# Performance work log

Measured on AMD Instinct MI355X. Metric: run time of the kernel, lower is better.

The kernel has to match this reference:

```python
import jax, jax.numpy as jnp
import numpy as np

INPUT_SIZE = 1024
HIDDEN_SIZE = 1024
SEQ_LEN = 512
BATCH = 64


def setup_inputs() -> dict:
    key = jax.random.key(0)
    ks = jax.random.split(key, 9)
    I, H = INPUT_SIZE, HIDDEN_SIZE
    s3 = 1.0 / np.sqrt(I + 2 * H)  # torch nn.Linear default init scale
    s2 = 1.0 / np.sqrt(I + H)
    return {
        "x": jax.random.normal(ks[0], (SEQ_LEN, BATCH, I), dtype=jnp.float32),
        "hidden": jnp.zeros((BATCH, H), dtype=jnp.float32),
        "cell": jnp.zeros((BATCH, H), dtype=jnp.float32),
        "W_write": jax.random.uniform(ks[1], (H, I + 2 * H), minval=-s3, maxval=s3),
        "b_write": jax.random.uniform(ks[2], (H,), minval=-s3, maxval=s3),
        "W_forget": jax.random.uniform(ks[3], (H, I + 2 * H), minval=-s3, maxval=s3),
        "b_forget": jax.random.uniform(ks[4], (H,), minval=-s3, maxval=s3),
        "W_cell": jax.random.uniform(ks[5], (H, I + H), minval=-s2, maxval=s2),
        "b_cell": jax.random.uniform(ks[6], (H,), minval=-s2, maxval=s2),
        "W_output": jax.random.uniform(ks[7], (H, I + 2 * H), minval=-s3, maxval=s3),
        "b_output": jax.random.uniform(ks[8], (H,), minval=-s3, maxval=s3),
    }


def reference(x, hidden, cell, W_write, b_write, W_forget, b_forget,
              W_cell, b_cell, W_output, b_output):
    # Peephole-style LSTM: write/forget gates see (x, h, c); candidate sees
    # (x, h); output gate sees (x, h, c_new). Sequential over time via scan.
    def step(carry, x_t):
        h, c = carry
        comb_xhc = jnp.concatenate([x_t, h, c], axis=-1)          # [B, I+2H]
        w = jax.nn.sigmoid(comb_xhc @ W_write.T + b_write)        # write gate
        f = jax.nn.sigmoid(comb_xhc @ W_forget.T + b_forget)      # forget gate
        comb_xh = jnp.concatenate([x_t, h], axis=-1)              # [B, I+H]
        c_new = f * c + w * jnp.tanh(comb_xh @ W_cell.T + b_cell)
        comb_new = jnp.concatenate([x_t, h, c_new], axis=-1)
        o = jax.nn.sigmoid(comb_new @ W_output.T + b_output)      # output gate
        h_new = o * jnp.tanh(c_new)
        return (h_new, c_new), h_new

    (h_f, c_f), outputs = jax.lax.scan(step, (hidden, cell), x)
    return outputs, (h_f, c_f)
```

## Files before the change

### kernel.cpp

```cpp
#include <hip/hip_runtime.h>
#include <hip/hip_bf16.h>
#include <stdint.h>


typedef __attribute__((ext_vector_type(8))) short short8;
typedef __attribute__((ext_vector_type(4))) float f32x4;
typedef __attribute__((ext_vector_type(4))) unsigned int uint4v;

#define OFF_WB   25165824u
#define OFF_HBF  27262976u
#define OFF_CBF  27525120u
#define OFF_BAR  27787264u
#define WS_NEED  27918336u

__device__ __forceinline__ short bfc(float f) {
  __hip_bfloat16 h = __float2bfloat16(f);
  return *reinterpret_cast<short*>(&h);
}
__device__ __forceinline__ unsigned pk2(float a, float b) {
  __hip_bfloat16 ha = __float2bfloat16(a), hb = __float2bfloat16(b);
  unsigned short ua = *reinterpret_cast<unsigned short*>(&ha);
  unsigned short ub = *reinterpret_cast<unsigned short*>(&hb);
  return (unsigned)ua | ((unsigned)ub << 16);
}
__device__ __forceinline__ float sig_fast(float v) {
  return __fdividef(1.f, 1.f + __expf(-v));
}
__device__ __forceinline__ float tanh_fast(float v) {
  float a = fabsf(v);
  float e = __expf(-2.f * a);
  float t = (1.f - e) * __fdividef(1.f, 1.f + e);
  return copysignf(t, v);
}

__device__ __forceinline__ uint4v ldg_sc(const void* p) {
  uint4v r;
  asm volatile("global_load_dwordx4 %0, %1, off sc0 sc1" : "=v"(r) : "v"(p));
  return r;
}
__device__ __forceinline__ unsigned poll_sc(const unsigned* p) {
  unsigned r;
  asm volatile("global_load_dword %0, %1, off sc0 sc1\n\ts_waitcnt vmcnt(0)"
               : "=v"(r) : "v"(p) : "memory");
  return r;
}
__device__ __forceinline__ void stg_u32_sc(unsigned* p, unsigned v) {
  asm volatile("global_store_dword %0, %1, off sc0 sc1" :: "v"(p), "v"(v) : "memory");
}

#define Z0 1310720LL
#define Z1 131072LL
#define Z2 32768LL
#define Z3 32768LL

__global__ __launch_bounds__(256)
void prep_kernel(const float* __restrict__ h0, const float* __restrict__ c0,
                 const float* __restrict__ Ww, const float* __restrict__ Wf,
                 const float* __restrict__ Wc, const float* __restrict__ Wo,
                 char* __restrict__ ws) {
  __hip_bfloat16* WA  = (__hip_bfloat16*)ws;
  __hip_bfloat16* WB  = (__hip_bfloat16*)(ws + OFF_WB);
  unsigned*     hbf32 = (unsigned*)(ws + OFF_HBF);
  unsigned*       bar = (unsigned*)(ws + OFF_BAR);

  const long long total = Z0 + Z1 + Z2 + Z3;
  for (long long idx = (long long)blockIdx.x * 256 + threadIdx.x; idx < total;
       idx += (long long)gridDim.x * 256) {
    if (idx < Z0) {
      int l  = (int)(idx & 63);
      int s  = (int)((idx >> 6) % 320);
      int cg = (int)(idx / (320 * 64));
      int g, kc;
      if (s < 96)       { g = 0; kc = s; }
      else if (s < 192) { g = 1; kc = s - 96; }
      else if (s < 256) { g = 2; kc = s - 192; }
      else              { g = 3; kc = s - 256; }
      int j  = cg * 16 + (l & 15);
      int kb = kc * 32 + ((l >> 4) << 3);
      const float* W; int rl;
      if (g == 0)      { W = Ww; rl = 3072; }
      else if (g == 1) { W = Wf; rl = 3072; }
      else if (g == 2) { W = Wc; rl = 2048; }
      else             { W = Wo; rl = 3072; }
      const float* src = W + (size_t)j * rl + kb;
      __hip_bfloat16* dst = WA + ((((size_t)cg * 4 + g) * 96 + kc) * 64 + l) * 8;
#pragma unroll
      for (int e = 0; e < 8; ++e) dst[e] = __float2bfloat16(src[e]);
    } else if (idx < Z0 + Z1) {
      long long q = idx - Z0;
      int l  = (int)(q & 63);
      int kc = (int)((q >> 6) & 7);
      int v  = (int)((q >> 9) & 3);
      int cg = (int)(q >> 11);
      int j  = cg * 16 + (l & 15);
      int k  = 2048 + v * 256 + kc * 32 + ((l >> 4) << 3);
      const float* src = Wo + (size_t)j * 3072 + k;
      __hip_bfloat16* dst = WB + ((((size_t)cg * 4 + v) * 8 + kc) * 64 + l) * 8;
#pragma unroll
      for (int e = 0; e < 8; ++e) dst[e] = __float2bfloat16(src[e]);
    } else if (idx < Z0 + Z1 + Z2) {
      int u  = (int)(idx - (Z0 + Z1));
      int R  = u >> 9, pp = u & 511;
      int cgp = pp >> 3, cprp = pp & 7;
      int dst = ((R >> 4) * 64 + cgp) * 128 + (R & 15) * 8 + cprp;
      const float* hs = h0 + (size_t)R * 1024 + 2 * pp;
      hbf32[dst] = pk2(hs[0], hs[1]);
    } else {
      int i = (int)(idx - (Z0 + Z1 + Z2));
      bar[i] = 0u;
    }
  }
}

__global__ __launch_bounds__(256, 1)
void lstm_kernel(const float* __restrict__ x,  const float* __restrict__ c0,
                 const float* __restrict__ bw, const float* __restrict__ bfg,
                 const float* __restrict__ bc, const float* __restrict__ bo,
                 float* __restrict__ out, char* __restrict__ ws) {
  char*     hbf   = ws + OFF_HBF;
  char*     cbf   = ws + OFF_CBF;
  unsigned* hflag = (unsigned*)(ws + OFF_BAR);
  unsigned* cflag = (unsigned*)(ws + OFF_BAR) + 4096;

  const int tid  = threadIdx.x;
  const int l    = tid & 63;
  const int wv   = tid >> 6;
  const int ks   = wv;
  const int b    = blockIdx.x;
  const int cg   = ((b & 7) << 3) | ((b >> 3) & 7);
  const int grp  = b >> 6;
  const int col  = l & 15;
  const int kg   = l >> 4;
  const int row16 = col;
  const int srow  = row16 & 7;

  const short8* BWb = (const short8*)ws + ((size_t)cg * 4) * 96 * 64 + l;
  const short8* BO  = (const short8*)(ws + OFF_WB) + ((size_t)(cg * 4 + wv)) * 8 * 64 + l;

  __shared__ __align__(16) char sx[32768];
  __shared__ __align__(16) char sc_[32768];
  __shared__ float lds[20][16][17];

  const int crow = tid >> 3;
  const int cpr  = tid & 7;
  const int coff = ((grp * 16 + crow) << 10) + (cg << 4) + 2 * cpr;
  float c_reg0 = 0.f, c_reg1 = 0.f;
  float bw0r = 0.f, bw1r = 0.f, bf0r = 0.f, bf1r = 0.f;
  float bc0r = 0.f, bc1r = 0.f, bo0r = 0.f, bo1r = 0.f;
  if (tid < 128) {
    c_reg0 = c0[coff]; c_reg1 = c0[coff + 1];
    int jc = (cg << 4) + 2 * cpr;
    bw0r = bw[jc];  bw1r = bw[jc + 1];
    bf0r = bfg[jc]; bf1r = bfg[jc + 1];
    bc0r = bc[jc];  bc1r = bc[jc + 1];
    bo0r = bo[jc];  bo1r = bo[jc + 1];
  }
  char* hDst = hbf + ((size_t)(grp * 64 + cg)) * 512 + crow * 32 + cpr * 4;
  char* cDst = cbf + ((size_t)(grp * 64 + cg)) * 512 + crow * 32 + cpr * 4;
  unsigned* hflagP = hflag + (grp * 64 + cg) * 16;
  unsigned* cflagP = cflag + (grp * 64 + cg) * 16;

  {
    const float* cs = c0 + (size_t)grp * 16384;
#pragma unroll
    for (int i = 0; i < 8; ++i) {
      int q = i * 256 + tid;
      const float* s = cs + q * 8;
      float4 f0 = *(const float4*)s;
      float4 f1 = *(const float4*)(s + 4);
      short8 v;
      v[0] = bfc(f0.x); v[1] = bfc(f0.y); v[2] = bfc(f0.z); v[3] = bfc(f0.w);
      v[4] = bfc(f1.x); v[5] = bfc(f1.y); v[6] = bfc(f1.z); v[7] = bfc(f1.w);
      int rw = q >> 7, kb = (q & 127) ^ (rw & 7);
      *(short8*)(sc_ + rw * 2048 + (kb << 4)) = v;
    }
  }
  {
    const float* xs = x + (size_t)grp * 16384;
#pragma unroll
    for (int i = 0; i < 8; ++i) {
      int q = i * 256 + tid;
      const float* s = xs + q * 8;
      float4 f0 = *(const float4*)s;
      float4 f1 = *(const float4*)(s + 4);
      short8 v;
      v[0] = bfc(f0.x); v[1] = bfc(f0.y); v[2] = bfc(f0.z); v[3] = bfc(f0.w);
      v[4] = bfc(f1.x); v[5] = bfc(f1.y); v[6] = bfc(f1.z); v[7] = bfc(f1.w);
      int rw = q >> 7, kb = (q & 127) ^ (rw & 7);
      *(short8*)(sx + rw * 2048 + (kb << 4)) = v;
    }
  }

  short8 WX[4][8];
#pragma unroll
  for (int g = 0; g < 4; ++g)
#pragma unroll
    for (int q = 0; q < 8; ++q)
      WX[g][q] = BWb[(size_t)(g * 96 + ks * 8 + q) * 64];
  short8 WC[2][8];
#pragma unroll
  for (int g = 0; g < 2; ++g)
#pragma unroll
    for (int q = 0; q < 8; ++q)
      WC[g][q] = BWb[(size_t)(g * 96 + 64 + ks * 8 + q) * 64];
  short8 WH[4][8];
#pragma unroll
  for (int g = 0; g < 4; ++g)
#pragma unroll
    for (int q = 0; q < 8; ++q)
      WH[g][q] = BWb[(size_t)(g * 96 + 32 + ks * 8 + q) * 64];
  short8 WBo[8];
#pragma unroll
  for (int k = 0; k < 8; ++k) WBo[k] = BO[(size_t)k * 64];

  __syncthreads();

  for (int t = 0; t < 512; ++t) {
    const int p = t & 1;
    const char* hslot = hbf + (size_t)p * 131072 + (size_t)grp * 32768;
    char* cslotW = cbf + (size_t)(p ^ 1) * 131072;

    __syncthreads();

    f32x4 acc[4][2];
#pragma unroll
    for (int g = 0; g < 4; ++g) {
      acc[g][0] = (f32x4){0.f, 0.f, 0.f, 0.f};
      acc[g][1] = (f32x4){0.f, 0.f, 0.f, 0.f};
    }

#pragma unroll
    for (int q = 0; q < 8; ++q) {
      int f = ks * 8 + q;
      short8 a = *(const short8*)(sx + row16 * 2048 + ((((f << 2) + kg) ^ srow) << 4));
      acc[0][q & 1] = __builtin_amdgcn_mfma_f32_16x16x32_bf16(a, WX[0][q], acc[0][q & 1], 0, 0, 0);
      acc[1][q & 1] = __builtin_amdgcn_mfma_f32_16x16x32_bf16(a, WX[1][q], acc[1][q & 1], 0, 0, 0);
      acc[2][q & 1] = __builtin_amdgcn_mfma_f32_16x16x32_bf16(a, WX[2][q], acc[2][q & 1], 0, 0, 0);
      acc[3][q & 1] = __builtin_amdgcn_mfma_f32_16x16x32_bf16(a, WX[3][q], acc[3][q & 1], 0, 0, 0);
    }
#pragma unroll
    for (int q = 0; q < 8; ++q) {
      int f = ks * 8 + q;
      short8 a = *(const short8*)(sc_ + row16 * 2048 + ((((f << 2) + kg) ^ srow) << 4));
      acc[0][q & 1] = __builtin_amdgcn_mfma_f32_16x16x32_bf16(a, WC[0][q], acc[0][q & 1], 0, 0, 0);
      acc[1][q & 1] = __builtin_amdgcn_mfma_f32_16x16x32_bf16(a, WC[1][q], acc[1][q & 1], 0, 0, 0);
    }

    if (l < 16) {
      const unsigned* pf = hflag + (grp * 64 + ks * 16 + l) * 16;
      const unsigned want = 2u * (unsigned)t;
      unsigned spins = 0;
      for (;;) {
        unsigned v = poll_sc(pf);
        if (__all((int)(v >= want))) break;
        __builtin_amdgcn_s_sleep(1);
        if (++spins > (1u << 18)) break;
      }
    }
    __builtin_amdgcn_sched_barrier(0);

    {
      const char* hb2 = hslot + row16 * 32 + (kg & 1) * 16;
      const int s0 = ks * 16 + (kg >> 1);
      uint4v ha[8];
#pragma unroll
      for (int q = 0; q < 8; ++q)
        ha[q] = ldg_sc(hb2 + (size_t)(s0 + 2 * q) * 512);
      asm volatile("s_waitcnt vmcnt(0)" ::: "memory");
      __builtin_amdgcn_sched_barrier(0);
#pragma unroll
      for (int q = 0; q < 8; ++q) {
        short8 a = __builtin_bit_cast(short8, ha[q]);
        acc[0][q & 1] = __builtin_amdgcn_mfma_f32_16x16x32_bf16(a, WH[0][q], acc[0][q & 1], 0, 0, 0);
        acc[1][q & 1] = __builtin_amdgcn_mfma_f32_16x16x32_bf16(a, WH[1][q], acc[1][q & 1], 0, 0, 0);
        acc[2][q & 1] = __builtin_amdgcn_mfma_f32_16x16x32_bf16(a, WH[2][q], acc[2][q & 1], 0, 0, 0);
        acc[3][q & 1] = __builtin_amdgcn_mfma_f32_16x16x32_bf16(a, WH[3][q], acc[3][q & 1], 0, 0, 0);
      }
    }
#pragma unroll
    for (int g = 0; g < 4; ++g)
#pragma unroll
      for (int i = 0; i < 4; ++i)
        lds[ks * 4 + g][kg * 4 + i][col] = acc[g][0][i] + acc[g][1][i];
    __syncthreads();

    if (tid < 128) {
      int c0i = 2 * cpr, c1i = 2 * cpr + 1;
      float aw0 = bw0r, aw1 = bw1r, af0 = bf0r, af1 = bf1r, ag0 = bc0r, ag1 = bc1r;
#pragma unroll
      for (int k = 0; k < 4; ++k) {
        aw0 += lds[k * 4 + 0][crow][c0i]; aw1 += lds[k * 4 + 0][crow][c1i];
        af0 += lds[k * 4 + 1][crow][c0i]; af1 += lds[k * 4 + 1][crow][c1i];
        ag0 += lds[k * 4 + 2][crow][c0i]; ag1 += lds[k * 4 + 2][crow][c1i];
      }
      float cn0 = sig_fast(af0) * c_reg0 + sig_fast(aw0) * tanh_fast(ag0);
      float cn1 = sig_fast(af1) * c_reg1 + sig_fast(aw1) * tanh_fast(ag1);
      c_reg0 = cn0; c_reg1 = cn1;
      stg_u32_sc((unsigned*)(cDst + (size_t)(p ^ 1) * 131072), pk2(cn0, cn1));
      asm volatile("s_waitcnt vmcnt(0)" ::: "memory");
      if (l == 0)
        __hip_atomic_fetch_add(cflagP, 1u,
                               __ATOMIC_RELAXED, __HIP_MEMORY_SCOPE_AGENT);
    }

    if (t < 511) {
      const float* xs = x + (((size_t)t + 1) << 16) + (size_t)grp * 16384;
#pragma unroll
      for (int i = 0; i < 8; ++i) {
        int q = i * 256 + tid;
        const float* s = xs + q * 8;
        float4 f0 = *(const float4*)s;
        float4 f1 = *(const float4*)(s + 4);
        short8 v;
        v[0] = bfc(f0.x); v[1] = bfc(f0.y); v[2] = bfc(f0.z); v[3] = bfc(f0.w);
        v[4] = bfc(f1.x); v[5] = bfc(f1.y); v[6] = bfc(f1.z); v[7] = bfc(f1.w);
        int rw = q >> 7, kb = (q & 127) ^ (rw & 7);
        *(short8*)(sx + rw * 2048 + (kb << 4)) = v;
      }
    }

    if (l < 16) {
      const unsigned* pf = cflag + (grp * 64 + wv * 16 + l) * 16;
      const unsigned want = 2u * ((unsigned)t + 1u);
      unsigned spins = 0;
      for (;;) {
        unsigned v = poll_sc(pf);
        if (__all((int)(v >= want))) break;
        __builtin_amdgcn_s_sleep(1);
        if (++spins > (1u << 18)) break;
      }
    }
    __builtin_amdgcn_sched_barrier(0);

    {
      const char* cslot = cslotW + (size_t)grp * 32768 + row16 * 32 + (kg & 1) * 16;
      uint4v ca[8];
#pragma unroll
      for (int kcc = 0; kcc < 8; ++kcc) {
        int s = wv * 16 + kcc * 2 + (kg >> 1);
        ca[kcc] = ldg_sc(cslot + (size_t)s * 512);
      }
      asm volatile("s_waitcnt vmcnt(0)" ::: "memory");
      __builtin_amdgcn_sched_barrier(0);
      f32x4 a0 = {0.f, 0.f, 0.f, 0.f}, a1 = {0.f, 0.f, 0.f, 0.f};
#pragma unroll
      for (int kcc = 0; kcc < 8; ++kcc) {
        short8 a = __builtin_bit_cast(short8, ca[kcc]);
        if (kcc & 1) a1 = __builtin_amdgcn_mfma_f32_16x16x32_bf16(a, WBo[kcc], a1, 0, 0, 0);
        else         a0 = __builtin_amdgcn_mfma_f32_16x16x32_bf16(a, WBo[kcc], a0, 0, 0, 0);
      }
      const int ub = wv * 32 + kg;
#pragma unroll
      for (int kcc = 0; kcc < 8; ++kcc)
        *(uint4v*)(sc_ + row16 * 2048 + (((ub + kcc * 4) ^ srow) << 4)) = ca[kcc];
#pragma unroll
      for (int i = 0; i < 4; ++i)
        lds[16 + wv][kg * 4 + i][col] = a0[i] + a1[i];
    }
    __syncthreads();

    if (tid < 128) {
      int c0i = 2 * cpr, c1i = 2 * cpr + 1;
      float s0 = bo0r, s1 = bo1r;
#pragma unroll
      for (int k = 0; k < 4; ++k) {
        s0 += lds[k * 4 + 3][crow][c0i] + lds[16 + k][crow][c0i];
        s1 += lds[k * 4 + 3][crow][c1i] + lds[16 + k][crow][c1i];
      }
      float o0 = sig_fast(s0), o1 = sig_fast(s1);
      float h0v = o0 * tanh_fast(c_reg0);
      float h1v = o1 * tanh_fast(c_reg1);
      stg_u32_sc((unsigned*)(hDst + (size_t)(p ^ 1) * 131072), pk2(h0v, h1v));
      asm volatile("s_waitcnt vmcnt(0)" ::: "memory");
      if (l == 0)
        __hip_atomic_fetch_add(hflagP, 1u,
                               __ATOMIC_RELAXED, __HIP_MEMORY_SCOPE_AGENT);
      float2 hv; hv.x = h0v; hv.y = h1v;
      *(float2*)(out + ((size_t)t << 16) + coff) = hv;
      if (t == 511) {
        *(float2*)(out + ((size_t)512 << 16) + coff) = hv;
        float2 cv; cv.x = c_reg0; cv.y = c_reg1;
        *(float2*)(out + ((size_t)512 << 16) + 65536 + coff) = cv;
      }
    }
  }
}

extern "C" void kernel_launch(void* const* d_in, const int* in_sizes, int n_in,
                              void* d_out, int out_size, void* d_ws, size_t ws_size,
                              hipStream_t stream) {
  (void)in_sizes; (void)n_in; (void)out_size;
  const float* x  = (const float*)d_in[0];
  const float* h0 = (const float*)d_in[1];
  const float* c0 = (const float*)d_in[2];
  const float* Ww = (const float*)d_in[3];
  const float* bw = (const float*)d_in[4];
  const float* Wf = (const float*)d_in[5];
  const float* bfg= (const float*)d_in[6];
  const float* Wc = (const float*)d_in[7];
  const float* bc = (const float*)d_in[8];
  const float* Wo = (const float*)d_in[9];
  const float* bo = (const float*)d_in[10];

  if (ws_size < (size_t)WS_NEED) return;

  prep_kernel<<<dim3(2048), dim3(256), 0, stream>>>(h0, c0, Ww, Wf, Wc, Wo,
                                                    (char*)d_ws);
  lstm_kernel<<<dim3(256), dim3(256), 0, stream>>>(x, c0, bw, bfg, bc, bo,
                                                   (float*)d_out, (char*)d_ws);
}
```

Measured before the change: 4.091 ms.

## Prefetch h/c flag probes early and split next-step x staging around the c wait

```diff
diff --git a/kernel.cpp b/kernel.cpp
--- a/kernel.cpp
+++ b/kernel.cpp
@@ -43,6 +43,9 @@
   asm volatile("global_load_dword %0, %1, off sc0 sc1\n\ts_waitcnt vmcnt(0)"
                : "=v"(r) : "v"(p) : "memory");
   return r;
+}
+__device__ __forceinline__ void probe_issue(const unsigned* p, unsigned& v) {
+  asm volatile("global_load_dword %0, %1, off sc0 sc1" : "=v"(v) : "v"(p));
 }
 __device__ __forceinline__ void stg_u32_sc(unsigned* p, unsigned v) {
   asm volatile("global_store_dword %0, %1, off sc0 sc1" :: "v"(p), "v"(v) : "memory");
@@ -159,6 +162,9 @@
   char* cDst = cbf + ((size_t)(grp * 64 + cg)) * 512 + crow * 32 + cpr * 4;
   unsigned* hflagP = hflag + (grp * 64 + cg) * 16;
   unsigned* cflagP = cflag + (grp * 64 + cg) * 16;
+  const unsigned* hprobe_p = hflag + (grp * 64 + ks * 16 + (l & 15)) * 16;
+  const unsigned* cprobe_p = cflag + (grp * 64 + ks * 16 + (l & 15)) * 16;
+  unsigned hprobe_v = 0u, cprobe_v = 0u;
 
   {
     const float* cs = c0 + (size_t)grp * 16384;
@@ -213,6 +219,8 @@
 #pragma unroll
   for (int k = 0; k < 8; ++k) WBo[k] = BO[(size_t)k * 64];
 
+  if (l < 16) probe_issue(hprobe_p, hprobe_v);
+
   __syncthreads();
 
   for (int t = 0; t < 512; ++t) {
@@ -247,14 +255,13 @@
     }
 
     if (l < 16) {
-      const unsigned* pf = hflag + (grp * 64 + ks * 16 + l) * 16;
       const unsigned want = 2u * (unsigned)t;
+      unsigned v = hprobe_v;
       unsigned spins = 0;
-      for (;;) {
-        unsigned v = poll_sc(pf);
-        if (__all((int)(v >= want))) break;
-        __builtin_amdgcn_s_sleep(1);
-        if (++spins > (1u << 18)) break;
+      while (!__all((int)(v >= want))) {
+        if (++spins > 2) __builtin_amdgcn_s_sleep(1);
+        if (spins > (1u << 18)) break;
+        v = poll_sc(hprobe_p);
       }
     }
     __builtin_amdgcn_sched_barrier(0);
@@ -302,11 +309,12 @@
         __hip_atomic_fetch_add(cflagP, 1u,
                                __ATOMIC_RELAXED, __HIP_MEMORY_SCOPE_AGENT);
     }
+    if (l < 16) probe_issue(cprobe_p, cprobe_v);
 
     if (t < 511) {
       const float* xs = x + (((size_t)t + 1) << 16) + (size_t)grp * 16384;
 #pragma unroll
-      for (int i = 0; i < 8; ++i) {
+      for (int i = 0; i < 4; ++i) {
         int q = i * 256 + tid;
         const float* s = xs + q * 8;
         float4 f0 = *(const float4*)s;
@@ -320,14 +328,13 @@
     }
 
     if (l < 16) {
-      const unsigned* pf = cflag + (grp * 64 + wv * 16 + l) * 16;
       const unsigned want = 2u * ((unsigned)t + 1u);
+      unsigned v = cprobe_v;
       unsigned spins = 0;
-      for (;;) {
-        unsigned v = poll_sc(pf);
-        if (__all((int)(v >= want))) break;
-        __builtin_amdgcn_s_sleep(1);
-        if (++spins > (1u << 18)) break;
+      while (!__all((int)(v >= want))) {
+        if (++spins > 2) __builtin_amdgcn_s_sleep(1);
+        if (spins > (1u << 18)) break;
+        v = poll_sc(cprobe_p);
       }
     }
     __builtin_amdgcn_sched_barrier(0);
@@ -383,6 +390,23 @@
         *(float2*)(out + ((size_t)512 << 16) + 65536 + coff) = cv;
       }
     }
+
+    if (t < 511) {
+      const float* xs = x + (((size_t)t + 1) << 16) + (size_t)grp * 16384;
+#pragma unroll
+      for (int i = 4; i < 8; ++i) {
+        int q = i * 256 + tid;
+        const float* s = xs + q * 8;
+        float4 f0 = *(const float4*)s;
+        float4 f1 = *(const float4*)(s + 4);
+        short8 v;
+        v[0] = bfc(f0.x); v[1] = bfc(f0.y); v[2] = bfc(f0.z); v[3] = bfc(f0.w);
+        v[4] = bfc(f1.x); v[5] = bfc(f1.y); v[6] = bfc(f1.z); v[7] = bfc(f1.w);
+        int rw = q >> 7, kb = (q & 127) ^ (rw & 7);
+        *(short8*)(sx + rw * 2048 + (kb << 4)) = v;
+      }
+    }
+    if (l < 16) probe_issue(hprobe_p, hprobe_v);
   }
 }
 
```

Result: slower. 4.270 ms (+4.4%).

## Replicate h/c exchange buffers and flags four ways to spread cross-block reads

Applied to the files above, without the earlier changes.

```diff
diff --git a/kernel.cpp b/kernel.cpp
--- a/kernel.cpp
+++ b/kernel.cpp
@@ -8,8 +8,9 @@
 typedef __attribute__((ext_vector_type(4))) unsigned int uint4v;
 
 #define OFF_WB   25165824u
-#define OFF_HBF  27262976u
-#define OFF_CBF  27525120u
+#define REP_H    23068672u
+#define REP_C    24117248u
+#define INIT_H   27262976u
 #define OFF_BAR  27787264u
 #define WS_NEED  27918336u
 
@@ -60,7 +61,7 @@
                  char* __restrict__ ws) {
   __hip_bfloat16* WA  = (__hip_bfloat16*)ws;
   __hip_bfloat16* WB  = (__hip_bfloat16*)(ws + OFF_WB);
-  unsigned*     hbf32 = (unsigned*)(ws + OFF_HBF);
+  unsigned*      initH = (unsigned*)(ws + INIT_H);
   unsigned*       bar = (unsigned*)(ws + OFF_BAR);
 
   const long long total = Z0 + Z1 + Z2 + Z3;
@@ -104,7 +105,9 @@
       int cgp = pp >> 3, cprp = pp & 7;
       int dst = ((R >> 4) * 64 + cgp) * 128 + (R & 15) * 8 + cprp;
       const float* hs = h0 + (size_t)R * 1024 + 2 * pp;
-      hbf32[dst] = pk2(hs[0], hs[1]);
+      unsigned pv = pk2(hs[0], hs[1]);
+#pragma unroll
+      for (int r = 0; r < 4; ++r) initH[r * 32768 + dst] = pv;
     } else {
       int i = (int)(idx - (Z0 + Z1 + Z2));
       bar[i] = 0u;
@@ -113,14 +116,19 @@
 }
 
 __global__ __launch_bounds__(256, 1)
-void lstm_kernel(const float* __restrict__ x,  const float* __restrict__ c0,
+void lstm_kernel(const float* __restrict__ x,  const float* __restrict__ h0,
+                 const float* __restrict__ c0,
                  const float* __restrict__ bw, const float* __restrict__ bfg,
                  const float* __restrict__ bc, const float* __restrict__ bo,
                  float* __restrict__ out, char* __restrict__ ws) {
-  char*     hbf   = ws + OFF_HBF;
-  char*     cbf   = ws + OFF_CBF;
-  unsigned* hflag = (unsigned*)(ws + OFF_BAR);
-  unsigned* cflag = (unsigned*)(ws + OFF_BAR) + 4096;
+  (void)h0;
+  char*     repH  = ws + REP_H;
+  char*     repC  = ws + REP_C;
+  char*     initH = ws + INIT_H;
+  unsigned* bar   = (unsigned*)(ws + OFF_BAR);
+  unsigned* hflag = bar;
+  unsigned* cflag = bar + 16384;
+  unsigned* ready = bar + 15;
 
   const int tid  = threadIdx.x;
   const int l    = tid & 63;
@@ -133,6 +141,7 @@
   const int kg   = l >> 4;
   const int row16 = col;
   const int srow  = row16 & 7;
+  const int myrep = cg & 3;
 
   const short8* BWb = (const short8*)ws + ((size_t)cg * 4) * 96 * 64 + l;
   const short8* BO  = (const short8*)(ws + OFF_WB) + ((size_t)(cg * 4 + wv)) * 8 * 64 + l;
@@ -155,10 +164,8 @@
     bc0r = bc[jc];  bc1r = bc[jc + 1];
     bo0r = bo[jc];  bo1r = bo[jc + 1];
   }
-  char* hDst = hbf + ((size_t)(grp * 64 + cg)) * 512 + crow * 32 + cpr * 4;
-  char* cDst = cbf + ((size_t)(grp * 64 + cg)) * 512 + crow * 32 + cpr * 4;
-  unsigned* hflagP = hflag + (grp * 64 + cg) * 16;
-  unsigned* cflagP = cflag + (grp * 64 + cg) * 16;
+  const size_t tileoff = (size_t)(grp * 64 + cg) * 512 + crow * 32 + cpr * 4;
+  const int flagoff = (grp * 64 + cg) * 16;
 
   {
     const float* cs = c0 + (size_t)grp * 16384;
@@ -213,12 +220,28 @@
 #pragma unroll
   for (int k = 0; k < 8; ++k) WBo[k] = BO[(size_t)k * 64];
 
+  asm volatile("s_waitcnt vmcnt(0)" ::: "memory");
+  __builtin_amdgcn_sched_barrier(0);
+  __syncthreads();
+  if (tid == 0) {
+    __hip_atomic_fetch_add(ready, 1u, __ATOMIC_RELAXED, __HIP_MEMORY_SCOPE_AGENT);
+    unsigned spins = 0;
+    for (;;) {
+      unsigned v = poll_sc(ready);
+      if (v >= 256u) break;
+      __builtin_amdgcn_s_sleep(1);
+      if (++spins > (1u << 18)) break;
+    }
+  }
   __syncthreads();
 
   for (int t = 0; t < 512; ++t) {
     const int p = t & 1;
-    const char* hslot = hbf + (size_t)p * 131072 + (size_t)grp * 32768;
-    char* cslotW = cbf + (size_t)(p ^ 1) * 131072;
+    const char* hslot = (t == 0)
+        ? (initH + (size_t)myrep * 131072 + (size_t)grp * 32768)
+        : (repH + (size_t)(myrep * 2 + p) * 131072 + (size_t)grp * 32768);
+    const char* cslotR = repC + (size_t)(myrep * 2 + (p ^ 1)) * 131072 +
+                         (size_t)grp * 32768;
 
     __syncthreads();
 
@@ -247,7 +270,7 @@
     }
 
     if (l < 16) {
-      const unsigned* pf = hflag + (grp * 64 + ks * 16 + l) * 16;
+      const unsigned* pf = hflag + myrep * 4096 + (grp * 64 + ks * 16 + l) * 16;
       const unsigned want = 2u * (unsigned)t;
       unsigned spins = 0;
       for (;;) {
@@ -296,11 +319,17 @@
       float cn0 = sig_fast(af0) * c_reg0 + sig_fast(aw0) * tanh_fast(ag0);
       float cn1 = sig_fast(af1) * c_reg1 + sig_fast(aw1) * tanh_fast(ag1);
       c_reg0 = cn0; c_reg1 = cn1;
-      stg_u32_sc((unsigned*)(cDst + (size_t)(p ^ 1) * 131072), pk2(cn0, cn1));
+      unsigned pkv = pk2(cn0, cn1);
+#pragma unroll
+      for (int r = 0; r < 4; ++r)
+        stg_u32_sc((unsigned*)(repC + (size_t)(r * 2 + (p ^ 1)) * 131072 + tileoff), pkv);
       asm volatile("s_waitcnt vmcnt(0)" ::: "memory");
-      if (l == 0)
-        __hip_atomic_fetch_add(cflagP, 1u,
-                               __ATOMIC_RELAXED, __HIP_MEMORY_SCOPE_AGENT);
+      if (l == 0) {
+#pragma unroll
+        for (int r = 0; r < 4; ++r)
+          __hip_atomic_fetch_add(cflag + r * 4096 + flagoff, 1u,
+                                 __ATOMIC_RELAXED, __HIP_MEMORY_SCOPE_AGENT);
+      }
     }
 
     if (t < 511) {
@@ -320,7 +349,7 @@
     }
 
     if (l < 16) {
-      const unsigned* pf = cflag + (grp * 64 + wv * 16 + l) * 16;
+      const unsigned* pf = cflag + myrep * 4096 + (grp * 64 + wv * 16 + l) * 16;
       const unsigned want = 2u * ((unsigned)t + 1u);
       unsigned spins = 0;
       for (;;) {
@@ -333,7 +362,7 @@
     __builtin_amdgcn_sched_barrier(0);
 
     {
-      const char* cslot = cslotW + (size_t)grp * 32768 + row16 * 32 + (kg & 1) * 16;
+      const char* cslot = cslotR + row16 * 32 + (kg & 1) * 16;
       uint4v ca[8];
 #pragma unroll
       for (int kcc = 0; kcc < 8; ++kcc) {
@@ -370,11 +399,17 @@
       float o0 = sig_fast(s0), o1 = sig_fast(s1);
       float h0v = o0 * tanh_fast(c_reg0);
       float h1v = o1 * tanh_fast(c_reg1);
-      stg_u32_sc((unsigned*)(hDst + (size_t)(p ^ 1) * 131072), pk2(h0v, h1v));
+      unsigned pkv = pk2(h0v, h1v);
+#pragma unroll
+      for (int r = 0; r < 4; ++r)
+        stg_u32_sc((unsigned*)(repH + (size_t)(r * 2 + (p ^ 1)) * 131072 + tileoff), pkv);
       asm volatile("s_waitcnt vmcnt(0)" ::: "memory");
-      if (l == 0)
-        __hip_atomic_fetch_add(hflagP, 1u,
-                               __ATOMIC_RELAXED, __HIP_MEMORY_SCOPE_AGENT);
+      if (l == 0) {
+#pragma unroll
+        for (int r = 0; r < 4; ++r)
+          __hip_atomic_fetch_add(hflag + r * 4096 + flagoff, 1u,
+                                 __ATOMIC_RELAXED, __HIP_MEMORY_SCOPE_AGENT);
+      }
       float2 hv; hv.x = h0v; hv.y = h1v;
       *(float2*)(out + ((size_t)t << 16) + coff) = hv;
       if (t == 511) {
@@ -406,6 +441,6 @@
 
   prep_kernel<<<dim3(2048), dim3(256), 0, stream>>>(h0, c0, Ww, Wf, Wc, Wo,
                                                     (char*)d_ws);
-  lstm_kernel<<<dim3(256), dim3(256), 0, stream>>>(x, c0, bw, bfg, bc, bo,
+  lstm_kernel<<<dim3(256), dim3(256), 0, stream>>>(x, h0, c0, bw, bfg, bc, bo,
                                                    (float*)d_out, (char*)d_ws);
 }
```

Result: slower. 4.276 ms (+4.5%).
